# Optimization experiments

Hardware: AMD Instinct MI355X
Metric: run time of the kernel (lower is better)

## Reference

```python
import jax, jax.numpy as jnp
from jax import lax
import numpy as np

B, L, NW, D, KS, TOPK, H = 32, 16384, 8000, 10, 22, 50, 2  # batch, seqlen, vocab, dim, conv kernel, top-k, heads
DN = ('NHWC', 'HWIO', 'NHWC')


def setup_inputs() -> dict:
    key = jax.random.key(0)
    ks = jax.random.split(key, 20)
    def n(i, shape, s=0.05):
        return jax.random.normal(ks[i], shape, jnp.float32) * s
    # tokens in [1, NW] -> no padding, so the ragged per-sample path is a dense batch
    inputs = jax.random.randint(ks[0], (B, 2, L), 1, NW + 1, dtype=jnp.int32)
    return {
        'inputs': inputs,
        'emb': n(1, (NW + 1, D), 0.1),            # Embedding(n_words+1, dim)
        'w1': n(2, (KS, KS, 1, 1)), 'b1': jnp.zeros((1,), jnp.float32),
        'w2': n(3, (KS, KS, 1, 1)), 'b2': jnp.zeros((1,), jnp.float32),
        'w3': n(4, (KS, KS, 1, 1)), 'b3': jnp.zeros((1,), jnp.float32),
        'wq': n(5, (D, H, D), 0.2), 'bq': jnp.zeros((H, D), jnp.float32),
        'wk': n(6, (D, H, D), 0.2), 'bk': jnp.zeros((H, D), jnp.float32),
        'wv': n(7, (D, H, D), 0.2), 'bv': jnp.zeros((H, D), jnp.float32),
        'wo': n(8, (H, D, D), 0.2), 'bo': jnp.zeros((D,), jnp.float32),
        'wf': n(9, (D, 2), 0.3), 'bf': jnp.zeros((2,), jnp.float32),
    }


def _encode(tok, emb, convs):
    x = emb[tok][..., None]                      # [B, L, D, 1] (NHWC, H=L, W=D)
    for w, b in convs:
        x = jax.nn.relu(lax.conv_general_dilated(x, w, (1, 1), 'SAME', dimension_numbers=DN) + b)
    x = jnp.transpose(x[..., 0], (0, 2, 1))      # [B, D, L]
    x = lax.top_k(x, TOPK)[0]                    # top-50 activations per channel
    return jnp.transpose(x, (0, 2, 1))           # [B, 50, D]


def _mha(q, kv, wq, bq, wk, bk, wv, bv, wo, bo):
    # keras MultiHeadAttention(num_heads=2, key_dim=D), key defaults to value
    Q = jnp.einsum('bqd,dhe->bqhe', q, wq) + bq
    K = jnp.einsum('bsd,dhe->bshe', kv, wk) + bk
    V = jnp.einsum('bsd,dhe->bshe', kv, wv) + bv
    logits = jnp.einsum('bqhe,bshe->bhqs', Q, K) / jnp.sqrt(jnp.float32(D))
    A = jax.nn.softmax(logits, axis=-1)
    O = jnp.einsum('bhqs,bshe->bqhe', A, V)
    return jnp.einsum('bqhe,hed->bqd', O, wo) + bo


def reference(inputs, emb, w1, b1, w2, b2, w3, b3, wq, bq, wk, bk, wv, bv, wo, bo, wf, bf):
    convs = ((w1, b1), (w2, b2), (w3, b3))
    f1 = _encode(inputs[:, 0], emb, convs)       # [B, 50, D]
    f2 = _encode(inputs[:, 1], emb, convs)
    r1 = jnp.sum(_mha(f1, f2, wq, bq, wk, bk, wv, bv, wo, bo), axis=1)  # [B, D]
    r2 = jnp.sum(_mha(f2, f1, wq, bq, wk, bk, wv, bv, wo, bo), axis=1)
    x = jnp.stack([r1, r2], axis=1)              # [B, 2, D]  (Concatenate axis=2 on [B,1,1,D])
    out = jax.nn.softmax(x @ wf + bf, axis=-1)   # [B, 2, 2]
    return out.reshape(-1, 2)                    # [2B, 2]
```

## Files before the change

### kernel.cpp

```cpp
#include <hip/hip_runtime.h>
#include <hip/hip_bf16.h>

#define LSEQ   16384
#define BATCH  32
#define NBS    64
#define NW     8000
#define CHUNK  448
#define NCHK   37
#define ROWS   536
#define RS     24

typedef short v8s __attribute__((ext_vector_type(8)));
typedef float v4f __attribute__((ext_vector_type(4)));
typedef _Float16 hf2 __attribute__((ext_vector_type(2)));

__device__ __forceinline__ unsigned short f2bf(float f) {
  unsigned u = __float_as_uint(f);
  unsigned r = u + 0x7FFFu + ((u >> 16) & 1u);
  return (unsigned short)(r >> 16);
}
__device__ __forceinline__ unsigned short cvt_bf16(float v) {
  __hip_bfloat16 hb = __float2bfloat16(v);
  unsigned short us;
  __builtin_memcpy(&us, &hb, 2);
  return us;
}

__global__ __launch_bounds__(256) void prep_kernel(
    const float* __restrict__ emb, const float* __restrict__ w1,
    const float* __restrict__ w2, const float* __restrict__ w3,
    unsigned short* __restrict__ emb16, unsigned short* __restrict__ bh) {
  int bid = blockIdx.x;
  if (bid < 32) {
    int r = bid * 256 + threadIdx.x;
    if (r > NW) return;
    const float2* er = reinterpret_cast<const float2*>(emb + r * 10);
    float v[10];
#pragma unroll
    for (int k = 0; k < 5; ++k) { float2 t2 = er[k]; v[2 * k] = t2.x; v[2 * k + 1] = t2.y; }
    v8s lo8 = (v8s)0, hi8 = (v8s)0;
#pragma unroll
    for (int j = 0; j < 8; ++j) lo8[j] = (short)f2bf(v[j]);
    hi8[0] = (short)f2bf(v[8]);
    hi8[1] = (short)f2bf(v[9]);
    v8s* dst = reinterpret_cast<v8s*>(emb16 + r * 16);
    dst[0] = lo8;
    dst[1] = hi8;
  } else {
    int idx = (bid - 32) * 256 + threadIdx.x;
    if (idx >= 3 * 11 * 64) return;
    int lane = idx & 63, rest = idx >> 6;
    int t = rest % 11, stage = rest / 11;
    const float* W = (stage == 0) ? w1 : (stage == 1) ? w2 : w3;
    int col = lane & 15;
    int kh = 2 * t + (lane >> 5);
    int wi0 = ((lane >> 4) & 1) * 8;
#pragma unroll
    for (int j = 0; j < 8; ++j) {
      int wi = wi0 + j;
      int kw = wi - col + 10;
      float v = (wi < 10 && col < 10 && kw >= 0 && kw < 22) ? W[kh * 22 + kw] : 0.0f;
      bh[idx * 8 + j] = f2bf(v);
    }
  }
}

__device__ __forceinline__ unsigned h2max_u(unsigned a, unsigned b) {
  hf2 r = __builtin_elementwise_max(__builtin_bit_cast(hf2, a),
                                    __builtin_bit_cast(hf2, b));
  return __builtin_bit_cast(unsigned, r);
}
__device__ __forceinline__ unsigned h2min_u(unsigned a, unsigned b) {
  hf2 r = __builtin_elementwise_min(__builtin_bit_cast(hf2, a),
                                    __builtin_bit_cast(hf2, b));
  return __builtin_bit_cast(unsigned, r);
}

__device__ __forceinline__ unsigned bsort64_h2(unsigned v, int lane) {
#pragma unroll
  for (int k = 2; k <= 64; k <<= 1) {
#pragma unroll
    for (int j = k >> 1; j > 0; j >>= 1) {
      unsigned o = __shfl_xor(v, j, 64);
      bool keepmax = (((lane & k) == 0) == ((lane & j) == 0));
      unsigned mx = h2max_u(v, o), mn = h2min_u(v, o);
      v = keepmax ? mx : mn;
    }
  }
  return v;
}
__device__ __forceinline__ unsigned bmerge64_h2(unsigned a, unsigned b, int lane) {
  unsigned rb = __shfl(b, 63 - lane, 64);
  unsigned m = h2max_u(a, rb);
#pragma unroll
  for (int j = 32; j > 0; j >>= 1) {
    unsigned o = __shfl_xor(m, j, 64);
    unsigned mx = h2max_u(m, o), mn = h2min_u(m, o);
    m = ((lane & j) == 0) ? mx : mn;
  }
  return m;
}

__global__ __launch_bounds__(512, 6) void conv_fused_kernel(
    const int* __restrict__ inputs, const unsigned short* __restrict__ emb16,
    const float* __restrict__ b1, const float* __restrict__ b2,
    const float* __restrict__ b3,
    const unsigned short* __restrict__ bh,
    unsigned* __restrict__ candp ) {
  __shared__ unsigned short plane[ROWS * RS];

  int blk = blockIdx.x;
  int bs = blk / NCHK;
  int chunk = blk - bs * NCHK;
  int base = chunk * CHUNK;
  int tid = threadIdx.x;
  int lane = tid & 63, wave = tid >> 6;

  const int* tokp = inputs + bs * LSEQ;
  for (int i = tid; i < ROWS; i += 512) {
    int seq = base - 32 + i;
    v8s lo8 = (v8s)0, hi8 = (v8s)0;
    if ((unsigned)seq < (unsigned)LSEQ) {
      int tok = tokp[seq];
      const v8s* er = reinterpret_cast<const v8s*>(emb16 + tok * 16);
      lo8 = er[0];
      hi8 = er[1];
    }
    *reinterpret_cast<v8s*>(&plane[i * RS + 0]) = lo8;
    *reinterpret_cast<v8s*>(&plane[i * RS + 8]) = hi8;
  }
  __syncthreads();

  const int laneA = ((lane & 15) + (lane >> 5) + 22) * RS + ((lane >> 4) & 1) * 8;
  const int col = lane & 15;
  const int rbase = (lane >> 4) * 4;

#pragma unroll 1
  for (int stage = 0; stage < 3; ++stage) {
    const int lo = (stage == 0) ? -20 : (stage == 1) ? -10 : 0;
    const int ntiles = (stage == 0) ? 32 : (stage == 1) ? 30 : 28;
    const float bias = (stage == 0) ? b1[0] : (stage == 1) ? b2[0] : b3[0];
    const int nt = (ntiles - wave + 7) >> 3;

    v4f acc[4];
#pragma unroll
    for (int m = 0; m < 4; ++m)
#pragma unroll
      for (int j = 0; j < 4; ++j) acc[m][j] = 0.0f;

    const v8s* bhf = reinterpret_cast<const v8s*>(bh) + (stage * 11) * 64 + lane;
    v8s bhc = bhf[0];

#pragma unroll 1
    for (int t = 0; t < 11; ++t) {
      v8s bhn = bhc;
      if (t < 10) bhn = bhf[(t + 1) * 64];
      const int toff = laneA + t * 2 * RS;
#pragma unroll
      for (int m = 0; m < 4; ++m) {
        if (m < nt) {
          int r0 = lo + (wave + 8 * m) * 16;
          v8s a = *reinterpret_cast<const v8s*>(&plane[toff + r0 * RS]);
          acc[m] = __builtin_amdgcn_mfma_f32_16x16x32_bf16(a, bhc, acc[m], 0, 0, 0);
        }
      }
      bhc = bhn;
    }
    __syncthreads();

#pragma unroll
    for (int m = 0; m < 4; ++m) {
      if (m < nt) {
        int r0 = lo + (wave + 8 * m) * 16;
#pragma unroll
        for (int j = 0; j < 4; ++j) {
          int rloc = r0 + rbase + j;
          int seq = base + rloc;
          unsigned short us = cvt_bf16(fmaxf(acc[m][j] + bias, 0.0f));
          bool ok = (col < 10) && ((unsigned)seq < (unsigned)LSEQ);
          plane[(rloc + 32) * RS + col] = ok ? us : (unsigned short)0;
        }
      }
    }
    __syncthreads();
  }

  if (wave < 5) {
    int p = wave;
    unsigned x[7];
#pragma unroll
    for (int s = 0; s < 7; ++s) {
      unsigned w = *reinterpret_cast<const unsigned*>(
          &plane[(32 + s * 64 + lane) * RS + 2 * p]);
      float flo = __uint_as_float(w << 16);
      float fhi = __uint_as_float(w & 0xFFFF0000u);
      hf2 h;
      h[0] = (_Float16)flo;
      h[1] = (_Float16)fhi;
      x[s] = __builtin_bit_cast(unsigned, h);
    }
#pragma unroll
    for (int s = 0; s < 7; ++s) x[s] = bsort64_h2(x[s], lane);
    unsigned y0 = bmerge64_h2(x[0], x[1], lane);
    unsigned y1 = bmerge64_h2(x[2], x[3], lane);
    unsigned y2 = bmerge64_h2(x[4], x[5], lane);
    unsigned z0 = bmerge64_h2(y0, y1, lane);
    unsigned z1 = bmerge64_h2(y2, x[6], lane);
    unsigned t  = bmerge64_h2(z0, z1, lane);
    if (lane < 50)
      candp[((bs * 5 + p) * NCHK + chunk) * 50 + lane] = t;
  }
}

__global__ __launch_bounds__(256) void merge_topk_kernel(
    const unsigned* __restrict__ candp, float* __restrict__ fbuf) {
  __shared__ unsigned ml[2048];
  int blk = blockIdx.x;
  int tid = threadIdx.x;
  const unsigned* src = candp + blk * (NCHK * 50);
  for (int i = tid; i < 2048; i += 256) ml[i] = (i < NCHK * 50) ? src[i] : 0u;
  for (int k = 2; k <= 2048; k <<= 1) {
    for (int j = k >> 1; j > 0; j >>= 1) {
      __syncthreads();
      for (int e = tid; e < 1024; e += 256) {
        int lo = ((e & ~(j - 1)) << 1) | (e & (j - 1));
        int hi = lo | j;
        unsigned a = ml[lo], b = ml[hi];
        bool desc = ((lo & k) == 0);
        unsigned mx = h2max_u(a, b), mn = h2min_u(a, b);
        ml[lo] = desc ? mx : mn;
        ml[hi] = desc ? mn : mx;
      }
    }
  }
  __syncthreads();
  if (tid < 50) {
    int bs = blk / 5, p = blk - bs * 5;
    hf2 h = __builtin_bit_cast(hf2, ml[tid]);
    fbuf[bs * 500 + tid * 10 + 2 * p + 0] = (float)h[0];
    fbuf[bs * 500 + tid * 10 + 2 * p + 1] = (float)h[1];
  }
}

__global__ __launch_bounds__(256) void mha_kernel(
    const float* __restrict__ fbuf,
    const float* __restrict__ wq, const float* __restrict__ bq,
    const float* __restrict__ wk, const float* __restrict__ bk,
    const float* __restrict__ wv, const float* __restrict__ bv,
    const float* __restrict__ wo, const float* __restrict__ bo,
    const float* __restrict__ wf, const float* __restrict__ bf,
    float* __restrict__ out) {
  __shared__ float f[2][50][10];
  __shared__ float Qm[50][2][10];
  __shared__ float Km[50][2][10];
  __shared__ float Vm[50][2][10];
  __shared__ float A2[2][50][50];
  __shared__ float Abar[2][50];
  __shared__ float OS[2][10];
  __shared__ float rr[10];

  int blk = blockIdx.x, b = blk >> 1, dir = blk & 1;
  int qs = dir, ks = dir ^ 1;
  int tid = threadIdx.x;

  for (int i = tid; i < 1000; i += 256) (&f[0][0][0])[i] = fbuf[b * 1000 + i];
  __syncthreads();

  for (int i = tid; i < 1000; i += 256) {
    int q = i / 20, rem = i - q * 20;
    int h = rem / 10, e = rem - h * 10;
    const float* fq = f[qs][q];
    const float* fk = f[ks][q];
    float aq = bq[h * 10 + e], ak = bk[h * 10 + e], av = bv[h * 10 + e];
#pragma unroll
    for (int dd = 0; dd < 10; ++dd) {
      int wIdx = dd * 20 + h * 10 + e;
      aq = fmaf(fq[dd], wq[wIdx], aq);
      ak = fmaf(fk[dd], wk[wIdx], ak);
      av = fmaf(fk[dd], wv[wIdx], av);
    }
    Qm[q][h][e] = aq; Km[q][h][e] = ak; Vm[q][h][e] = av;
  }
  __syncthreads();

  for (int row = tid; row < 100; row += 256) {
    int h = row / 50, q = row - h * 50;
    const float* Qr = Qm[q][h];
    float lg[50], m = -1e30f;
#pragma unroll
    for (int s = 0; s < 50; ++s) {
      const float* Kr = Km[s][h];
      float t = 0.0f;
#pragma unroll
      for (int e = 0; e < 10; ++e) t = fmaf(Qr[e], Kr[e], t);
      t *= 0.31622776601683794f;
      lg[s] = t; m = fmaxf(m, t);
    }
    float sum = 0.0f;
#pragma unroll
    for (int s = 0; s < 50; ++s) { float p = __expf(lg[s] - m); lg[s] = p; sum += p; }
    float inv = 1.0f / sum;
#pragma unroll
    for (int s = 0; s < 50; ++s) A2[h][q][s] = lg[s] * inv;
  }
  __syncthreads();

  for (int i = tid; i < 100; i += 256) {
    int h = i / 50, s = i - h * 50;
    float t = 0.0f;
#pragma unroll
    for (int q = 0; q < 50; ++q) t += A2[h][q][s];
    Abar[h][s] = t;
  }
  __syncthreads();
  if (tid < 20) {
    int h = tid / 10, e = tid - h * 10;
    float t = 0.0f;
#pragma unroll
    for (int s = 0; s < 50; ++s) t += Abar[h][s] * Vm[s][h][e];
    OS[h][e] = t;
  }
  __syncthreads();
  if (tid < 10) {
    int dc = tid;
    float t = 50.0f * bo[dc];
#pragma unroll
    for (int h = 0; h < 2; ++h)
#pragma unroll
      for (int e = 0; e < 10; ++e) t = fmaf(OS[h][e], wo[h * 100 + e * 10 + dc], t);
    rr[dc] = t;
  }
  __syncthreads();
  if (tid == 0) {
    float l0 = bf[0], l1 = bf[1];
#pragma unroll
    for (int dd = 0; dd < 10; ++dd) {
      l0 = fmaf(rr[dd], wf[dd * 2 + 0], l0);
      l1 = fmaf(rr[dd], wf[dd * 2 + 1], l1);
    }
    float m = fmaxf(l0, l1);
    float e0 = expf(l0 - m), e1 = expf(l1 - m);
    float inv = 1.0f / (e0 + e1);
    out[(b * 2 + dir) * 2 + 0] = e0 * inv;
    out[(b * 2 + dir) * 2 + 1] = e1 * inv;
  }
}

extern "C" void kernel_launch(void* const* d_in, const int* in_sizes, int n_in,
                              void* d_out, int out_size, void* d_ws, size_t ws_size,
                              hipStream_t stream) {
  const int*   inputs = (const int*)d_in[0];
  const float* emb = (const float*)d_in[1];
  const float* w1 = (const float*)d_in[2];
  const float* b1 = (const float*)d_in[3];
  const float* w2 = (const float*)d_in[4];
  const float* b2 = (const float*)d_in[5];
  const float* w3 = (const float*)d_in[6];
  const float* b3 = (const float*)d_in[7];
  const float* wq = (const float*)d_in[8];
  const float* bq = (const float*)d_in[9];
  const float* wk = (const float*)d_in[10];
  const float* bk = (const float*)d_in[11];
  const float* wv = (const float*)d_in[12];
  const float* bv = (const float*)d_in[13];
  const float* wo = (const float*)d_in[14];
  const float* bo = (const float*)d_in[15];
  const float* wf = (const float*)d_in[16];
  const float* bf = (const float*)d_in[17];
  float* out = (float*)d_out;

  float* fbuf = (float*)d_ws;
  unsigned* candp = (unsigned*)((float*)d_ws + 32768);
  unsigned short* bh = (unsigned short*)((float*)d_ws + 1216768);
  unsigned short* emb16 = bh + 16896;

  hipLaunchKernelGGL(prep_kernel, dim3(41), dim3(256), 0, stream,
                     emb, w1, w2, w3, emb16, bh);
  hipLaunchKernelGGL(conv_fused_kernel, dim3(NBS * NCHK), dim3(512), 0, stream,
                     inputs, emb16, b1, b2, b3, bh, candp);
  hipLaunchKernelGGL(merge_topk_kernel, dim3(NBS * 5), dim3(256), 0, stream, candp, fbuf);
  hipLaunchKernelGGL(mha_kernel, dim3(NBS), dim3(256), 0, stream,
                     fbuf, wq, bq, wk, bk, wv, bv, wo, bo, wf, bf, out);
}
```

Before: 122.8 us.

## Pack conv plane with 12-short row stride and fold K into 9 MFMA steps

```diff
diff --git a/kernel.cpp b/kernel.cpp
--- a/kernel.cpp
+++ b/kernel.cpp
@@ -8,9 +8,11 @@
 #define CHUNK  448
 #define NCHK   37
 #define ROWS   536
-#define RS     24
+#define RSW    12
+#define NT9    9
 
 typedef short v8s __attribute__((ext_vector_type(8)));
+typedef short v4s __attribute__((ext_vector_type(4)));
 typedef float v4f __attribute__((ext_vector_type(4)));
 typedef _Float16 hf2 __attribute__((ext_vector_type(2)));
 
@@ -48,18 +50,18 @@
     dst[1] = hi8;
   } else {
     int idx = (bid - 32) * 256 + threadIdx.x;
-    if (idx >= 3 * 11 * 64) return;
+    if (idx >= 3 * NT9 * 64) return;
     int lane = idx & 63, rest = idx >> 6;
-    int t = rest % 11, stage = rest / 11;
+    int t = rest % NT9, stage = rest / NT9;
     const float* W = (stage == 0) ? w1 : (stage == 1) ? w2 : w3;
     int col = lane & 15;
-    int kh = 2 * t + (lane >> 5);
-    int wi0 = ((lane >> 4) & 1) * 8;
 #pragma unroll
     for (int j = 0; j < 8; ++j) {
-      int wi = wi0 + j;
+      int k = 32 * t + 8 * (lane >> 4) + j;
+      int kh = k / 12, wi = k - 12 * kh;
       int kw = wi - col + 10;
-      float v = (wi < 10 && col < 10 && kw >= 0 && kw < 22) ? W[kh * 22 + kw] : 0.0f;
+      float v = (wi < 10 && col < 10 && kh < 22 && kw >= 0 && kw < 22)
+                    ? W[kh * 22 + kw] : 0.0f;
       bh[idx * 8 + j] = f2bf(v);
     }
   }
@@ -75,7 +77,6 @@
                                     __builtin_bit_cast(hf2, b));
   return __builtin_bit_cast(unsigned, r);
 }
-
 __device__ __forceinline__ unsigned bsort64_h2(unsigned v, int lane) {
 #pragma unroll
   for (int k = 2; k <= 64; k <<= 1) {
@@ -107,7 +108,7 @@
     const float* __restrict__ b3,
     const unsigned short* __restrict__ bh,
     unsigned* __restrict__ candp ) {
-  __shared__ unsigned short plane[ROWS * RS];
+  __shared__ unsigned short plane[ROWS * RSW];
 
   int blk = blockIdx.x;
   int bs = blk / NCHK;
@@ -119,21 +120,21 @@
   const int* tokp = inputs + bs * LSEQ;
   for (int i = tid; i < ROWS; i += 512) {
     int seq = base - 32 + i;
-    v8s lo8 = (v8s)0, hi8 = (v8s)0;
+    v4s a0 = (v4s)0, a1 = (v4s)0, a2 = (v4s)0;
     if ((unsigned)seq < (unsigned)LSEQ) {
       int tok = tokp[seq];
-      const v8s* er = reinterpret_cast<const v8s*>(emb16 + tok * 16);
-      lo8 = er[0];
-      hi8 = er[1];
-    }
-    *reinterpret_cast<v8s*>(&plane[i * RS + 0]) = lo8;
-    *reinterpret_cast<v8s*>(&plane[i * RS + 8]) = hi8;
-  }
-  __syncthreads();
-
-  const int laneA = ((lane & 15) + (lane >> 5) + 22) * RS + ((lane >> 4) & 1) * 8;
+      const v4s* er = reinterpret_cast<const v4s*>(emb16 + tok * 16);
+      a0 = er[0]; a1 = er[1]; a2 = er[2];
+    }
+    *reinterpret_cast<v4s*>(&plane[i * RSW + 0]) = a0;
+    *reinterpret_cast<v4s*>(&plane[i * RSW + 4]) = a1;
+    *reinterpret_cast<v4s*>(&plane[i * RSW + 8]) = a2;
+  }
+  __syncthreads();
+
+  const int laneA = ((lane & 15) + 22) * RSW + 8 * (lane >> 4);
   const int col = lane & 15;
-  const int rbase = (lane >> 4) * 4;
+  const int rbase = ((lane >> 4) & 3) * 4;
 
 #pragma unroll 1
   for (int stage = 0; stage < 3; ++stage) {
@@ -148,19 +149,24 @@
 #pragma unroll
       for (int j = 0; j < 4; ++j) acc[m][j] = 0.0f;
 
-    const v8s* bhf = reinterpret_cast<const v8s*>(bh) + (stage * 11) * 64 + lane;
+    const v8s* bhf = reinterpret_cast<const v8s*>(bh) + (stage * NT9) * 64 + lane;
     v8s bhc = bhf[0];
 
 #pragma unroll 1
-    for (int t = 0; t < 11; ++t) {
+    for (int t = 0; t < NT9; ++t) {
       v8s bhn = bhc;
-      if (t < 10) bhn = bhf[(t + 1) * 64];
-      const int toff = laneA + t * 2 * RS;
+      if (t < NT9 - 1) bhn = bhf[(t + 1) * 64];
+      const int toff = laneA + t * 32;
 #pragma unroll
       for (int m = 0; m < 4; ++m) {
         if (m < nt) {
           int r0 = lo + (wave + 8 * m) * 16;
-          v8s a = *reinterpret_cast<const v8s*>(&plane[toff + r0 * RS]);
+          int off = toff + r0 * RSW;
+          v4s alo = *reinterpret_cast<const v4s*>(&plane[off]);
+          v4s ahi = *reinterpret_cast<const v4s*>(&plane[off + 4]);
+          v8s a;
+#pragma unroll
+          for (int q = 0; q < 4; ++q) { a[q] = alo[q]; a[4 + q] = ahi[q]; }
           acc[m] = __builtin_amdgcn_mfma_f32_16x16x32_bf16(a, bhc, acc[m], 0, 0, 0);
         }
       }
@@ -178,7 +184,8 @@
           int seq = base + rloc;
           unsigned short us = cvt_bf16(fmaxf(acc[m][j] + bias, 0.0f));
           bool ok = (col < 10) && ((unsigned)seq < (unsigned)LSEQ);
-          plane[(rloc + 32) * RS + col] = ok ? us : (unsigned short)0;
+          if (col < 12)
+            plane[(rloc + 32) * RSW + col] = ok ? us : (unsigned short)0;
         }
       }
     }
@@ -191,7 +198,7 @@
 #pragma unroll
     for (int s = 0; s < 7; ++s) {
       unsigned w = *reinterpret_cast<const unsigned*>(
-          &plane[(32 + s * 64 + lane) * RS + 2 * p]);
+          &plane[(32 + s * 64 + lane) * RSW + 2 * p]);
       float flo = __uint_as_float(w << 16);
       float fhi = __uint_as_float(w & 0xFFFF0000u);
       hf2 h;
@@ -372,9 +379,9 @@
   float* fbuf = (float*)d_ws;
   unsigned* candp = (unsigned*)((float*)d_ws + 32768);
   unsigned short* bh = (unsigned short*)((float*)d_ws + 1216768);
-  unsigned short* emb16 = bh + 16896;
-
-  hipLaunchKernelGGL(prep_kernel, dim3(41), dim3(256), 0, stream,
+  unsigned short* emb16 = bh + 16384;
+
+  hipLaunchKernelGGL(prep_kernel, dim3(39), dim3(256), 0, stream,
                      emb, w1, w2, w3, emb16, bh);
   hipLaunchKernelGGL(conv_fused_kernel, dim3(NBS * NCHK), dim3(512), 0, stream,
                      inputs, emb16, b1, b2, b3, bh, candp);
```

After: 256.6 us. +109.0%, slower.

## Fuse top-k candidate merge into MHA kernel using wave-level bitonic merges

Applied to the files above, without the earlier changes.

```diff
diff --git a/kernel.cpp b/kernel.cpp
--- a/kernel.cpp
+++ b/kernel.cpp
@@ -75,7 +75,6 @@
                                     __builtin_bit_cast(hf2, b));
   return __builtin_bit_cast(unsigned, r);
 }
-
 __device__ __forceinline__ unsigned bsort64_h2(unsigned v, int lane) {
 #pragma unroll
   for (int k = 2; k <= 64; k <<= 1) {
@@ -212,38 +211,8 @@
   }
 }
 
-__global__ __launch_bounds__(256) void merge_topk_kernel(
-    const unsigned* __restrict__ candp, float* __restrict__ fbuf) {
-  __shared__ unsigned ml[2048];
-  int blk = blockIdx.x;
-  int tid = threadIdx.x;
-  const unsigned* src = candp + blk * (NCHK * 50);
-  for (int i = tid; i < 2048; i += 256) ml[i] = (i < NCHK * 50) ? src[i] : 0u;
-  for (int k = 2; k <= 2048; k <<= 1) {
-    for (int j = k >> 1; j > 0; j >>= 1) {
-      __syncthreads();
-      for (int e = tid; e < 1024; e += 256) {
-        int lo = ((e & ~(j - 1)) << 1) | (e & (j - 1));
-        int hi = lo | j;
-        unsigned a = ml[lo], b = ml[hi];
-        bool desc = ((lo & k) == 0);
-        unsigned mx = h2max_u(a, b), mn = h2min_u(a, b);
-        ml[lo] = desc ? mx : mn;
-        ml[hi] = desc ? mn : mx;
-      }
-    }
-  }
-  __syncthreads();
-  if (tid < 50) {
-    int bs = blk / 5, p = blk - bs * 5;
-    hf2 h = __builtin_bit_cast(hf2, ml[tid]);
-    fbuf[bs * 500 + tid * 10 + 2 * p + 0] = (float)h[0];
-    fbuf[bs * 500 + tid * 10 + 2 * p + 1] = (float)h[1];
-  }
-}
-
 __global__ __launch_bounds__(256) void mha_kernel(
-    const float* __restrict__ fbuf,
+    const unsigned* __restrict__ candp,
     const float* __restrict__ wq, const float* __restrict__ bq,
     const float* __restrict__ wk, const float* __restrict__ bk,
     const float* __restrict__ wv, const float* __restrict__ bv,
@@ -262,8 +231,24 @@
   int blk = blockIdx.x, b = blk >> 1, dir = blk & 1;
   int qs = dir, ks = dir ^ 1;
   int tid = threadIdx.x;
-
-  for (int i = tid; i < 1000; i += 256) (&f[0][0][0])[i] = fbuf[b * 1000 + i];
+  int lane = tid & 63, wave = tid >> 6;
+
+  for (int s = wave; s < 10; s += 4) {
+    int s2 = s / 5, p = s - s2 * 5;
+    int bs = 2 * b + s2;
+    const unsigned* src = candp + ((bs * 5 + p) * NCHK) * 50;
+    unsigned acc = (lane < 50) ? src[lane] : 0u;
+#pragma unroll 1
+    for (int c = 1; c < NCHK; ++c) {
+      unsigned cur = (lane < 50) ? src[c * 50 + lane] : 0u;
+      acc = bmerge64_h2(acc, cur, lane);
+    }
+    if (lane < 50) {
+      hf2 h = __builtin_bit_cast(hf2, acc);
+      f[s2][lane][2 * p + 0] = (float)h[0];
+      f[s2][lane][2 * p + 1] = (float)h[1];
+    }
+  }
   __syncthreads();
 
   for (int i = tid; i < 1000; i += 256) {
@@ -369,7 +354,6 @@
   const float* bf = (const float*)d_in[17];
   float* out = (float*)d_out;
 
-  float* fbuf = (float*)d_ws;
   unsigned* candp = (unsigned*)((float*)d_ws + 32768);
   unsigned short* bh = (unsigned short*)((float*)d_ws + 1216768);
   unsigned short* emb16 = bh + 16896;
@@ -378,7 +362,6 @@
                      emb, w1, w2, w3, emb16, bh);
   hipLaunchKernelGGL(conv_fused_kernel, dim3(NBS * NCHK), dim3(512), 0, stream,
                      inputs, emb16, b1, b2, b3, bh, candp);
-  hipLaunchKernelGGL(merge_topk_kernel, dim3(NBS * 5), dim3(256), 0, stream, candp, fbuf);
   hipLaunchKernelGGL(mha_kernel, dim3(NBS), dim3(256), 0, stream,
-                     fbuf, wq, bq, wk, bk, wv, bv, wo, bo, wf, bf, out);
-}
+                     candp, wq, bq, wk, bk, wv, bv, wo, bo, wf, bf, out);
+}
```

New measurement: 147.6 us. 20.2% more time.
